# Kernel tuning notes

Hardware: AMD Instinct MI355X
Metric: run time of the kernel (lower is better)

The kernel has to match this reference:

```python
import jax, jax.numpy as jnp
import numpy as np

N, L, H, E = 4, 2048, 8, 64
S, D = 2048, 64
EPS = 1e-6

def setup_inputs() -> dict:
    key = jax.random.key(0)
    k1, k2, k3 = jax.random.split(key, 3)
    return {
        "queries": jax.random.normal(k1, (N, L, H, E), dtype=jnp.float32),
        "keys": jax.random.normal(k2, (N, S, H, E), dtype=jnp.float32),
        "values": jax.random.normal(k3, (N, S, H, D), dtype=jnp.float32),
        "key_mask": jnp.ones((N, S), dtype=jnp.float32),
    }

def reference(queries, keys, values, key_mask):
    n, l, h, e = queries.shape
    _, s, _, d = values.shape
    softmax_temp = 1.0 / np.sqrt(e).astype(np.float32)
    # Faithful to torch: .view(N,H,L,E) is a reshape of the contiguous
    # (N,L,H,E) buffer, NOT a transpose.
    q = queries.reshape(n, h, l, e)
    k = keys.reshape(n, h, s, e)
    # squared euclidean distance ||q_i - k_j||^2 via expansion (== cdist^2)
    q_sq = jnp.sum(q * q, axis=-1)  # [n,h,l]
    k_sq = jnp.sum(k * k, axis=-1)  # [n,h,s]
    qk = jnp.einsum('nhle,nhse->nhls', q, k)
    dist_sq = jnp.maximum(q_sq[..., :, None] + k_sq[..., None, :] - 2.0 * qk, 0.0)
    phi = jnp.exp(-softmax_temp * (dist_sq * 0.5))  # [n,h,l,s]
    phi = phi * key_mask[:, None, None, :]
    Z = 1.0 / (jnp.sum(phi, axis=-1) + EPS)  # [n,h,l]
    out = jnp.einsum('nhls,nshd,nhl->nlhd', phi, values, Z)
    return out
```

## Files before the change

kernel.cpp:

```cpp
#include <hip/hip_runtime.h>
#include <stdint.h>


#define N_ 4
#define L_ 2048
#define H_ 8
#define S_ 2048

#define C1 0.18033688f
#define C2 0.09016844f

typedef unsigned short ushort_t;
typedef unsigned int uint_t;
typedef __bf16 b8 __attribute__((ext_vector_type(8)));
typedef float f4 __attribute__((ext_vector_type(4)));
typedef const __attribute__((address_space(1))) uint32_t* gas_ptr;
typedef __attribute__((address_space(3))) uint32_t* las_ptr;

static __device__ __forceinline__ ushort_t f2bf(float x) {
  uint32_t u = __float_as_uint(x);
  u += 0x7fffu + ((u >> 16) & 1u);
  return (ushort_t)(u >> 16);
}

__global__ __launch_bounds__(256) void k_prep(const float* __restrict__ ksrc,
                                              ushort_t* __restrict__ kdst,
                                              float* __restrict__ lbf,
                                              const float* __restrict__ mask,
                                              const float* __restrict__ v,
                                              ushort_t* __restrict__ vt) {
  __shared__ __align__(16) ushort_t tile[64][68];
  if (blockIdx.x < 1024) {
    int t = blockIdx.x * 256 + threadIdx.x;
    int row = t >> 2, part = t & 3;
    const float4* p = reinterpret_cast<const float4*>(ksrc + (size_t)row * 64 + part * 16);
    uint_t o[8];
    float s = 0.f;
#pragma unroll
    for (int i = 0; i < 4; ++i) {
      float4 vv = p[i];
      s += vv.x * vv.x + vv.y * vv.y + vv.z * vv.z + vv.w * vv.w;
      o[2 * i]     = (uint_t)f2bf(vv.x) | ((uint_t)f2bf(vv.y) << 16);
      o[2 * i + 1] = (uint_t)f2bf(vv.z) | ((uint_t)f2bf(vv.w) << 16);
    }
    uint4* dp = reinterpret_cast<uint4*>(kdst + (size_t)row * 64 + part * 16);
    dp[0] = make_uint4(o[0], o[1], o[2], o[3]);
    dp[1] = make_uint4(o[4], o[5], o[6], o[7]);
    s += __shfl_xor(s, 1);
    s += __shfl_xor(s, 2);
    if (part == 0) {
      int n = row >> 14;
      int sidx = row & (S_ - 1);
      float m = mask[n * S_ + sidx];
      lbf[row] = -C2 * s + __log2f(m);
    }
  } else {
    const int vb = blockIdx.x - 1024;
    const int sc = vb & 31;
    const int h = (vb >> 5) & 7;
    const int n = vb >> 8;
    const int t = threadIdx.x;
    const int sl = t >> 4;
    const int dp = (t & 15) * 4;
#pragma unroll
    for (int i = 0; i < 4; ++i) {
      int s = sc * 64 + i * 16 + sl;
      float4 val = *reinterpret_cast<const float4*>(
          v + (((size_t)n * S_ + s) * H_ + h) * 64 + dp);
      tile[dp + 0][i * 16 + sl] = f2bf(val.x);
      tile[dp + 1][i * 16 + sl] = f2bf(val.y);
      tile[dp + 2][i * 16 + sl] = f2bf(val.z);
      tile[dp + 3][i * 16 + sl] = f2bf(val.w);
    }
    __syncthreads();
    const int d = t >> 2, sp = (t & 3) * 16;
    uint_t o[8];
#pragma unroll
    for (int i = 0; i < 8; ++i) {
      const int p0 = sp + 2 * i, p1 = p0 + 1;
      const int s0 = (p0 & 32) + (((p0 >> 2) & 1) << 4) + (((p0 >> 3) & 3) << 2) + (p0 & 3);
      const int s1 = (p1 & 32) + (((p1 >> 2) & 1) << 4) + (((p1 >> 3) & 3) << 2) + (p1 & 3);
      o[i] = (uint_t)tile[d][s0] | ((uint_t)tile[d][s1] << 16);
    }
    size_t base = ((size_t)(n * H_ + h) * 64 + d) * S_ + sc * 64 + sp;
    uint4* w = reinterpret_cast<uint4*>(vt + base);
    w[0] = make_uint4(o[0], o[1], o[2], o[3]);
    w[1] = make_uint4(o[4], o[5], o[6], o[7]);
  }
}

__global__ __launch_bounds__(256, 4) void k_attn(
    const float* __restrict__ qf32, const ushort_t* __restrict__ kb,
    const ushort_t* __restrict__ vt, const float* __restrict__ lbf,
    float* __restrict__ out) {
  __shared__ __align__(16) ushort_t kt[2][64 * 64];
  __shared__ __align__(16) ushort_t vtt[2][64 * 64];
  __shared__ __align__(16) float zb[4][16];

  const int lane = threadIdx.x & 63;
  const int w = threadIdx.x >> 6;
  const int bid = blockIdx.x;
  const int swz = (bid & 7) * 128 + (bid >> 3);
  const int qt = swz & 31;
  const int hd = (swz >> 5) & 7;
  const int n = swz >> 8;
  const int nh = n * H_ + hd;
  const int c = lane & 15;
  const int g = lane >> 4;
  const int qrow0 = qt * 64 + w * 16;

  union U4 { uint_t u[4]; b8 v; };

  const float* qsrc = qf32 + ((size_t)nh * L_ + qrow0) * 64;
  b8 qfr[2];
  float epsr;
  {
    const float* rp = qsrc + (size_t)c * 64 + g * 8;
    float s = 0.f;
#pragma unroll
    for (int es = 0; es < 2; ++es) {
      float4 v0 = *reinterpret_cast<const float4*>(rp + es * 32);
      float4 v1 = *reinterpret_cast<const float4*>(rp + es * 32 + 4);
      s += v0.x * v0.x + v0.y * v0.y + v0.z * v0.z + v0.w * v0.w
         + v1.x * v1.x + v1.y * v1.y + v1.z * v1.z + v1.w * v1.w;
      U4 tq;
      tq.u[0] = (uint_t)f2bf(v0.x) | ((uint_t)f2bf(v0.y) << 16);
      tq.u[1] = (uint_t)f2bf(v0.z) | ((uint_t)f2bf(v0.w) << 16);
      tq.u[2] = (uint_t)f2bf(v1.x) | ((uint_t)f2bf(v1.y) << 16);
      tq.u[3] = (uint_t)f2bf(v1.z) | ((uint_t)f2bf(v1.w) << 16);
      qfr[es] = tq.v;
    }
    s += __shfl_xor(s, 16);
    s += __shfl_xor(s, 32);
    epsr = 1e-6f * exp2f(C2 * s);
  }

  const ushort_t* kbh = kb + (size_t)nh * S_ * 64;
  const ushort_t* vth = vt + (size_t)nh * 64 * S_;
  const float* lbh = lbf + (size_t)nh * S_;

  f4 zero4 = {0.f, 0.f, 0.f, 0.f};
  f4 acc[4] = {zero4, zero4, zero4, zero4};
  float rs = 0.f;

  const int lrow = lane >> 3;
  const int lc16 = (lane & 7) ^ lrow;

  float4 lbA[4], lbB[4];

#define WAITV8 asm volatile("s_waitcnt vmcnt(8)" ::: "memory")
#define WAITV4 asm volatile("s_waitcnt vmcnt(4)" ::: "memory")

#define STAGE(bufi, ch)                                                        \
  {                                                                            \
    _Pragma("unroll")                                                          \
    for (int t2 = 0; t2 < 2; ++t2) {                                           \
      const int rr = w * 16 + t2 * 8;                                          \
      const ushort_t* gk = kbh + ((size_t)(ch) * 64 + rr + lrow) * 64 + lc16 * 8; \
      __builtin_amdgcn_global_load_lds((gas_ptr)gk, (las_ptr)(&kt[bufi][rr * 64]), 16, 0, 0); \
      const ushort_t* gv = vth + (size_t)(rr + lrow) * S_ + (ch) * 64 + lc16 * 8; \
      __builtin_amdgcn_global_load_lds((gas_ptr)gv, (las_ptr)(&vtt[bufi][rr * 64]), 16, 0, 0); \
    }                                                                          \
  }

#define LBLOAD(dst, ch)                                                        \
  {                                                                            \
    _Pragma("unroll")                                                          \
    for (int ss = 0; ss < 4; ++ss)                                             \
      dst[ss] = *reinterpret_cast<const float4*>(lbh + (ch) * 64 + ss * 16 + 4 * g); \
  }

#define CHUNK(CH, BUF, LBC, LBN, DO_LB, DO_S, WAITX)                           \
  {                                                                            \
    WAITX;                                                                     \
    __builtin_amdgcn_s_barrier();                                              \
    __builtin_amdgcn_sched_barrier(0);                                         \
    uint_t pw[8];                                                              \
    _Pragma("unroll")                                                          \
    for (int ss = 0; ss < 4; ++ss) {                                           \
      const ushort_t* ktb = &kt[BUF][(ss * 16 + c) * 64];                      \
      b8 ak0 = *reinterpret_cast<const b8*>(ktb + (g ^ (c & 7)) * 8);          \
      b8 ak1 = *reinterpret_cast<const b8*>(ktb + ((4 + g) ^ (c & 7)) * 8);    \
      __builtin_amdgcn_s_setprio(1);                                           \
      f4 s0 = __builtin_amdgcn_mfma_f32_16x16x32_bf16(ak0, qfr[0], zero4, 0, 0, 0); \
      s0 = __builtin_amdgcn_mfma_f32_16x16x32_bf16(ak1, qfr[1], s0, 0, 0, 0);  \
      __builtin_amdgcn_s_setprio(0);                                           \
      float p0 = exp2f(fmaf(C1, s0[0], LBC[ss].x));                            \
      float p1 = exp2f(fmaf(C1, s0[1], LBC[ss].y));                            \
      float p2 = exp2f(fmaf(C1, s0[2], LBC[ss].z));                            \
      float p3 = exp2f(fmaf(C1, s0[3], LBC[ss].w));                            \
      rs += (p0 + p1) + (p2 + p3);                                             \
      asm("v_cvt_pk_bf16_f32 %0, %1, %2" : "=v"(pw[2 * ss])     : "v"(p0), "v"(p1)); \
      asm("v_cvt_pk_bf16_f32 %0, %1, %2" : "=v"(pw[2 * ss + 1]) : "v"(p2), "v"(p3)); \
    }                                                                          \
    __builtin_amdgcn_s_setprio(1);                                             \
    _Pragma("unroll")                                                          \
    for (int sst = 0; sst < 2; ++sst) {                                        \
      U4 pa;                                                                   \
      pa.u[0] = pw[4 * sst + 0]; pa.u[1] = pw[4 * sst + 1];                    \
      pa.u[2] = pw[4 * sst + 2]; pa.u[3] = pw[4 * sst + 3];                    \
      _Pragma("unroll")                                                        \
      for (int db = 0; db < 4; ++db) {                                         \
        b8 bv = *reinterpret_cast<const b8*>(                                  \
            &vtt[BUF][(db * 16 + c) * 64] + (((4 * sst + g) ^ (c & 7)) * 8));  \
        acc[db] = __builtin_amdgcn_mfma_f32_16x16x32_bf16(pa.v, bv, acc[db], 0, 0, 0); \
      }                                                                        \
    }                                                                          \
    __builtin_amdgcn_s_setprio(0);                                             \
    __builtin_amdgcn_sched_barrier(0);                                         \
    __builtin_amdgcn_s_barrier();                                              \
    if (DO_LB) { LBLOAD(LBN, (CH) + 1); }                                      \
    __builtin_amdgcn_sched_barrier(0);                                         \
    if (DO_S) { STAGE(BUF, (CH) + 2); }                                        \
  }

  STAGE(0, 0);
  LBLOAD(lbA, 0);
  __builtin_amdgcn_sched_barrier(0);
  STAGE(1, 1);

  for (int ch = 0; ch < 28; ch += 2) {
    CHUNK(ch,     0, lbA, lbB, true, true, WAITV8);
    CHUNK(ch + 1, 1, lbB, lbA, true, true, WAITV8);
  }
  CHUNK(28, 0, lbA, lbB, true,  true,  WAITV8);
  CHUNK(29, 1, lbB, lbA, true,  true,  WAITV8);
  CHUNK(30, 0, lbA, lbB, true,  false, WAITV8);
  CHUNK(31, 1, lbB, lbA, false, false, WAITV4);

#undef CHUNK
#undef STAGE
#undef LBLOAD
#undef WAITV8
#undef WAITV4

  rs += __shfl_xor(rs, 16);
  rs += __shfl_xor(rs, 32);
  if (g == 0) zb[w][c] = 1.f / (rs + epsr);
  __syncthreads();

  const float4 z4 = *reinterpret_cast<const float4*>(&zb[w][4 * g]);
  const float zz[4] = {z4.x, z4.y, z4.z, z4.w};
  float* ob = out + (((size_t)n * L_ + qrow0 + 4 * g) * H_ + hd) * 64;
#pragma unroll
  for (int db = 0; db < 4; ++db) {
#pragma unroll
    for (int r = 0; r < 4; ++r) {
      ob[(size_t)r * (H_ * 64) + db * 16 + c] = acc[db][r] * zz[r];
    }
  }
}

extern "C" void kernel_launch(void* const* d_in, const int* in_sizes, int n_in,
                              void* d_out, int out_size, void* d_ws, size_t ws_size,
                              hipStream_t stream) {
  const float* q = (const float*)d_in[0];
  const float* k = (const float*)d_in[1];
  const float* v = (const float*)d_in[2];
  const float* mask = (const float*)d_in[3];
  float* out = (float*)d_out;

  char* ws = (char*)d_ws;
  ushort_t* kb = (ushort_t*)ws;
  ushort_t* vt = (ushort_t*)(ws + ((size_t)8 << 20));
  float* lbf = (float*)(ws + ((size_t)16 << 20));

  k_prep<<<dim3(2048), dim3(256), 0, stream>>>(k, kb, lbf, mask, v, vt);
  k_attn<<<dim3(1024), dim3(256), 0, stream>>>(q, kb, vt, lbf, out);
}
```

Measured before the change: 77.18 us.

## Load V fragments directly into registers instead of staging through LDS

Drops the LDS double buffer for V. Each wave now loads its V B-operand fragments straight from global memory into registers for the next chunk, and the double-buffered bias registers become a single buffer. Launch bounds drop from 4 to 2 blocks per CU to make room for the extra registers, and the vmcnt wait thresholds change to match the new load counts. This removes LDS traffic and the LDS footprint for V, but the four waves of a block each load the same V tile, and next-chunk loads are issued only one chunk ahead, so global latency is less well hidden and occupancy is lower.

```diff
diff --git a/kernel.cpp b/kernel.cpp
--- a/kernel.cpp
+++ b/kernel.cpp
@@ -89,12 +89,11 @@
   }
 }
 
-__global__ __launch_bounds__(256, 4) void k_attn(
+__global__ __launch_bounds__(256, 2) void k_attn(
     const float* __restrict__ qf32, const ushort_t* __restrict__ kb,
     const ushort_t* __restrict__ vt, const float* __restrict__ lbf,
     float* __restrict__ out) {
   __shared__ __align__(16) ushort_t kt[2][64 * 64];
-  __shared__ __align__(16) ushort_t vtt[2][64 * 64];
   __shared__ __align__(16) float zb[4][16];
 
   const int lane = threadIdx.x & 63;
@@ -146,10 +145,16 @@
   const int lrow = lane >> 3;
   const int lc16 = (lane & 7) ^ lrow;
 
-  float4 lbA[4], lbB[4];
-
-#define WAITV8 asm volatile("s_waitcnt vmcnt(8)" ::: "memory")
-#define WAITV4 asm volatile("s_waitcnt vmcnt(4)" ::: "memory")
+  float4 lbv[4];
+  b8 vf[8];
+
+  const ushort_t* vp0 = vth + (size_t)(0 * 16 + c) * S_ + g * 8;
+  const ushort_t* vp1 = vth + (size_t)(1 * 16 + c) * S_ + g * 8;
+  const ushort_t* vp2 = vth + (size_t)(2 * 16 + c) * S_ + g * 8;
+  const ushort_t* vp3 = vth + (size_t)(3 * 16 + c) * S_ + g * 8;
+
+#define WAITV14 asm volatile("s_waitcnt vmcnt(14)" ::: "memory")
+#define WAITV12 asm volatile("s_waitcnt vmcnt(12)" ::: "memory")
 
 #define STAGE(bufi, ch)                                                        \
   {                                                                            \
@@ -158,19 +163,29 @@
       const int rr = w * 16 + t2 * 8;                                          \
       const ushort_t* gk = kbh + ((size_t)(ch) * 64 + rr + lrow) * 64 + lc16 * 8; \
       __builtin_amdgcn_global_load_lds((gas_ptr)gk, (las_ptr)(&kt[bufi][rr * 64]), 16, 0, 0); \
-      const ushort_t* gv = vth + (size_t)(rr + lrow) * S_ + (ch) * 64 + lc16 * 8; \
-      __builtin_amdgcn_global_load_lds((gas_ptr)gv, (las_ptr)(&vtt[bufi][rr * 64]), 16, 0, 0); \
     }                                                                          \
   }
 
-#define LBLOAD(dst, ch)                                                        \
+#define LBLOAD(ch)                                                             \
   {                                                                            \
     _Pragma("unroll")                                                          \
     for (int ss = 0; ss < 4; ++ss)                                             \
-      dst[ss] = *reinterpret_cast<const float4*>(lbh + (ch) * 64 + ss * 16 + 4 * g); \
-  }
-
-#define CHUNK(CH, BUF, LBC, LBN, DO_LB, DO_S, WAITX)                           \
+      lbv[ss] = *reinterpret_cast<const float4*>(lbh + (ch) * 64 + ss * 16 + 4 * g); \
+  }
+
+#define VLOAD(ch)                                                              \
+  {                                                                            \
+    vf[0] = *reinterpret_cast<const b8*>(vp0 + (ch) * 64);                     \
+    vf[1] = *reinterpret_cast<const b8*>(vp1 + (ch) * 64);                     \
+    vf[2] = *reinterpret_cast<const b8*>(vp2 + (ch) * 64);                     \
+    vf[3] = *reinterpret_cast<const b8*>(vp3 + (ch) * 64);                     \
+    vf[4] = *reinterpret_cast<const b8*>(vp0 + (ch) * 64 + 32);                \
+    vf[5] = *reinterpret_cast<const b8*>(vp1 + (ch) * 64 + 32);                \
+    vf[6] = *reinterpret_cast<const b8*>(vp2 + (ch) * 64 + 32);                \
+    vf[7] = *reinterpret_cast<const b8*>(vp3 + (ch) * 64 + 32);                \
+  }
+
+#define CHUNK(CH, BUF, DO_LB, DO_S, WAITX)                                     \
   {                                                                            \
     WAITX;                                                                     \
     __builtin_amdgcn_s_barrier();                                              \
@@ -185,10 +200,10 @@
       f4 s0 = __builtin_amdgcn_mfma_f32_16x16x32_bf16(ak0, qfr[0], zero4, 0, 0, 0); \
       s0 = __builtin_amdgcn_mfma_f32_16x16x32_bf16(ak1, qfr[1], s0, 0, 0, 0);  \
       __builtin_amdgcn_s_setprio(0);                                           \
-      float p0 = exp2f(fmaf(C1, s0[0], LBC[ss].x));                            \
-      float p1 = exp2f(fmaf(C1, s0[1], LBC[ss].y));                            \
-      float p2 = exp2f(fmaf(C1, s0[2], LBC[ss].z));                            \
-      float p3 = exp2f(fmaf(C1, s0[3], LBC[ss].w));                            \
+      float p0 = exp2f(fmaf(C1, s0[0], lbv[ss].x));                            \
+      float p1 = exp2f(fmaf(C1, s0[1], lbv[ss].y));                            \
+      float p2 = exp2f(fmaf(C1, s0[2], lbv[ss].z));                            \
+      float p3 = exp2f(fmaf(C1, s0[3], lbv[ss].w));                            \
       rs += (p0 + p1) + (p2 + p3);                                             \
       asm("v_cvt_pk_bf16_f32 %0, %1, %2" : "=v"(pw[2 * ss])     : "v"(p0), "v"(p1)); \
       asm("v_cvt_pk_bf16_f32 %0, %1, %2" : "=v"(pw[2 * ss + 1]) : "v"(p2), "v"(p3)); \
@@ -201,38 +216,38 @@
       pa.u[2] = pw[4 * sst + 2]; pa.u[3] = pw[4 * sst + 3];                    \
       _Pragma("unroll")                                                        \
       for (int db = 0; db < 4; ++db) {                                         \
-        b8 bv = *reinterpret_cast<const b8*>(                                  \
-            &vtt[BUF][(db * 16 + c) * 64] + (((4 * sst + g) ^ (c & 7)) * 8));  \
-        acc[db] = __builtin_amdgcn_mfma_f32_16x16x32_bf16(pa.v, bv, acc[db], 0, 0, 0); \
+        acc[db] = __builtin_amdgcn_mfma_f32_16x16x32_bf16(pa.v, vf[4 * sst + db], acc[db], 0, 0, 0); \
       }                                                                        \
     }                                                                          \
     __builtin_amdgcn_s_setprio(0);                                             \
     __builtin_amdgcn_sched_barrier(0);                                         \
     __builtin_amdgcn_s_barrier();                                              \
-    if (DO_LB) { LBLOAD(LBN, (CH) + 1); }                                      \
+    if (DO_LB) { LBLOAD((CH) + 1); VLOAD((CH) + 1); }                          \
     __builtin_amdgcn_sched_barrier(0);                                         \
     if (DO_S) { STAGE(BUF, (CH) + 2); }                                        \
   }
 
   STAGE(0, 0);
-  LBLOAD(lbA, 0);
+  LBLOAD(0);
+  VLOAD(0);
   __builtin_amdgcn_sched_barrier(0);
   STAGE(1, 1);
 
   for (int ch = 0; ch < 28; ch += 2) {
-    CHUNK(ch,     0, lbA, lbB, true, true, WAITV8);
-    CHUNK(ch + 1, 1, lbB, lbA, true, true, WAITV8);
-  }
-  CHUNK(28, 0, lbA, lbB, true,  true,  WAITV8);
-  CHUNK(29, 1, lbB, lbA, true,  true,  WAITV8);
-  CHUNK(30, 0, lbA, lbB, true,  false, WAITV8);
-  CHUNK(31, 1, lbB, lbA, false, false, WAITV4);
+    CHUNK(ch,     0, true, true, WAITV14);
+    CHUNK(ch + 1, 1, true, true, WAITV14);
+  }
+  CHUNK(28, 0, true,  true,  WAITV14);
+  CHUNK(29, 1, true,  true,  WAITV14);
+  CHUNK(30, 0, true,  false, WAITV14);
+  CHUNK(31, 1, false, false, WAITV12);
 
 #undef CHUNK
 #undef STAGE
 #undef LBLOAD
-#undef WAITV8
-#undef WAITV4
+#undef VLOAD
+#undef WAITV14
+#undef WAITV12
 
   rs += __shfl_xor(rs, 16);
   rs += __shfl_xor(rs, 32);
```

After: 190.7 us. +147.1%, slower.
